# Kernel tuning notes

Hardware: AMD Instinct MI355X
Metric: run time of the kernel (lower is better)

Reference implementation:

```python
import jax, jax.numpy as jnp
import numpy as np

K_NEIGHBORS = 16  # matches init kwarg k


def _knn_idx(x, K):
    # x: (b, n, 3). Full pairwise squared distances, then top-K smallest.
    sq = jnp.sum(x * x, axis=-1)                                   # (b, n)
    d2 = sq[:, :, None] + sq[:, None, :] - 2.0 * jnp.einsum('bnc,bmc->bnm', x, x)
    _, idx = jax.lax.top_k(-d2, K)                                  # nearest first (includes self)
    return idx                                                      # (b, n, K)


def _gather(points, idx):
    # points: (b, n, C), idx: (b, n, K) -> (b, n, K, C)
    return jax.vmap(lambda p, i: p[i])(points, idx)


def _kappa_std(pc, normal, k):
    # pc, normal: (b, 3, n)
    x = pc.transpose(0, 2, 1)        # (b, n, 3)
    nrm = normal.transpose(0, 2, 1)  # (b, n, 3)
    idx = _knn_idx(x, k + 1)         # (b, n, k+1)
    nn_pts = _gather(x, idx)[:, :, 1:, :]          # drop self -> (b, n, k, 3)
    v = nn_pts - x[:, :, None, :]                   # (b, n, k, 3)
    v = v / jnp.clip(jnp.linalg.norm(v, axis=-1, keepdims=True), 1e-12)
    kappa = jnp.abs(jnp.sum(v * nrm[:, :, None, :], axis=-1)).mean(axis=-1)  # (b, n)
    nn_kappa = _gather(kappa[..., None], idx)[:, :, 1:, 0]                    # (b, n, k)
    # torch.std default: unbiased (ddof=1)
    return jnp.std(nn_kappa, axis=-1, ddof=1)                                  # (b, n)


def setup_inputs() -> dict:
    key = jax.random.key(0)
    k1, k2, k3 = jax.random.split(key, 3)
    b, n = 4, 4096
    ori_data = jax.random.normal(k1, (b, 3, n), dtype=jnp.float32)
    adv_data = ori_data + 0.05 * jax.random.normal(k2, (b, 3, n), dtype=jnp.float32)
    nrm = jax.random.normal(k3, (b, 3, n), dtype=jnp.float32)
    ori_normal = nrm / jnp.clip(jnp.linalg.norm(nrm, axis=1, keepdims=True), 1e-12)
    return {"ori_data": ori_data, "adv_data": adv_data, "ori_normal": ori_normal}


def reference(ori_data, adv_data, ori_normal):
    k = K_NEIGHBORS
    ori_std = _kappa_std(ori_data, ori_normal, k)   # (b, n)
    adv_std = _kappa_std(adv_data, ori_normal, k)   # (b, n)
    # torch PairwiseDistance(p=2, eps=1e-6): ||x1 - x2 + eps||_2 over last dim
    dist = jnp.linalg.norm(ori_std - adv_std + 1e-6, axis=-1)  # (b,)
    return dist.mean()
```

## Files before the change

kernel.cpp:

```cpp
#include <hip/hip_runtime.h>
#include <math.h>

#define NPTS 4096
#define BATCH 4
#define KNB 16
#define BIG 3.0e38f
#define CAP 1024

__device__ __forceinline__ void bsort_stage(float& d, int& s, int lane, int k, int j) {
  const float od = __shfl_xor(d, j);
  const int   os = __shfl_xor(s, j);
  const bool keepMin = ((lane & k) == 0) == ((lane & j) == 0);
  const bool takeO = keepMin ? (od < d) : (od > d);
  d = takeO ? od : d;
  s = takeO ? os : s;
}

__device__ __forceinline__ void bitonic_sort64(float& d, int& s, int lane) {
#pragma unroll
  for (int k = 2; k <= 64; k <<= 1) {
#pragma unroll
    for (int j = k >> 1; j >= 1; j >>= 1)
      bsort_stage(d, s, lane, k, j);
  }
}

__device__ __forceinline__ void bitonic_merge64(float& d, int& s, int lane) {
#pragma unroll
  for (int j = 32; j >= 1; j >>= 1)
    bsort_stage(d, s, lane, 64, j);
}

__device__ __forceinline__ void bitonic_sort64_v(float& d, int lane) {
#pragma unroll
  for (int k = 2; k <= 64; k <<= 1) {
#pragma unroll
    for (int j = k >> 1; j >= 1; j >>= 1) {
      const float od = __shfl_xor(d, j);
      const bool keepMin = ((lane & k) == 0) == ((lane & j) == 0);
      d = keepMin ? fminf(d, od) : fmaxf(d, od);
    }
  }
}

__global__ __launch_bounds__(256)
void knn_kappa_kernel(const float* __restrict__ ori,
                      const float* __restrict__ adv,
                      const float* __restrict__ nrm,
                      float* __restrict__ kappaWs,
                      int* __restrict__ idxWs) {
  const int i    = blockIdx.x;
  const int b    = blockIdx.y;
  const int ds   = blockIdx.z;
  const int t    = threadIdx.x;
  const int lane = t & 63;
  const int w    = t >> 6;

  const float* __restrict__ P  = (ds == 0 ? ori : adv) + (size_t)b * 3 * NPTS;
  const float* __restrict__ Xp = P;
  const float* __restrict__ Yp = P + NPTS;
  const float* __restrict__ Zp = P + 2 * NPTS;

  __shared__ float candD[CAP];
  __shared__ int   candI[CAP];
  __shared__ float wTau[4];
  __shared__ unsigned int cnt;

  if (t == 0) cnt = 0;

  const float xi = Xp[i], yi = Yp[i], zi = Zp[i];

  float d[16];
  float tmin = BIG;
#pragma unroll
  for (int u = 0; u < 16; ++u) {
    const int j = u * 256 + t;
    const float dx = Xp[j] - xi;
    const float dy = Yp[j] - yi;
    const float dz = Zp[j] - zi;
    float d2 = fmaf(dx, dx, fmaf(dy, dy, dz * dz));
    if (j == i) d2 = BIG;
    d[u] = d2;
    tmin = fminf(tmin, d2);
  }

  float sm = tmin;
  bitonic_sort64_v(sm, lane);
  if (lane == (KNB - 1)) wTau[w] = sm;
  __syncthreads();
  const float tau = fminf(fminf(wTau[0], wTau[1]), fminf(wTau[2], wTau[3]));

#pragma unroll
  for (int u = 0; u < 16; ++u) {
    if (d[u] <= tau) {
      const unsigned pos = atomicAdd(&cnt, 1u);
      if (pos < CAP) { candD[pos] = d[u]; candI[pos] = u * 256 + t; }
    }
  }
  __syncthreads();

  if (w == 0) {
    const int M = (int)(cnt < CAP ? cnt : CAP);
    float sd = (lane < M) ? candD[lane] : BIG;
    int   si = (lane < M) ? lane : -1;
    bitonic_sort64(sd, si, lane);
    for (int c0 = 64; c0 < M; c0 += 64) {
      const int slot = c0 + lane;
      float vd = (slot < M) ? candD[slot] : BIG;
      int   vi = (slot < M) ? slot : -1;
      bitonic_sort64(vd, vi, lane);
      const float rd = __shfl_xor(vd, 63);
      const int   ri = __shfl_xor(vi, 63);
      if (rd < sd) { sd = rd; si = ri; }
      bitonic_merge64(sd, si, lane);
    }

    if (lane < KNB) {
      const int nbj = candI[si];
      const float px = Xp[nbj], py = Yp[nbj], pz = Zp[nbj];
      const float vx = px - xi, vy = py - yi, vz = pz - zi;
      float L = sqrtf(fmaf(vx, vx, fmaf(vy, vy, vz * vz)));
      L = fmaxf(L, 1e-12f);
      const float* __restrict__ nb_ = nrm + (size_t)b * 3 * NPTS;
      const float nx = nb_[i], ny = nb_[NPTS + i], nz = nb_[2 * NPTS + i];
      float c = fabsf(fmaf(vx, nx, fmaf(vy, ny, vz * nz)) / L);
      c += __shfl_xor(c, 1);
      c += __shfl_xor(c, 2);
      c += __shfl_xor(c, 4);
      c += __shfl_xor(c, 8);
      const size_t row = (size_t)(ds * BATCH + b) * NPTS + i;
      if (lane == 0) kappaWs[row] = c * (1.0f / 16.0f);
      idxWs[row * KNB + lane] = nbj;
    }
  }
}

__global__ __launch_bounds__(256)
void std_dist_kernel(const float* __restrict__ kappaWs,
                     const int* __restrict__ idxWs,
                     float* __restrict__ partial) {
  const int i = blockIdx.x * 256 + threadIdx.x;
  const int b = blockIdx.y;

  float s[2];
#pragma unroll
  for (int ds = 0; ds < 2; ++ds) {
    const size_t kb = (size_t)(ds * BATCH + b) * NPTS;
    const int* __restrict__ ip = idxWs + (kb + i) * KNB;
    float kv[16];
    float sum = 0.f;
#pragma unroll
    for (int u = 0; u < 16; ++u) {
      kv[u] = kappaWs[kb + ip[u]];
      sum += kv[u];
    }
    const float mean = sum * (1.0f / 16.0f);
    float ss = 0.f;
#pragma unroll
    for (int u = 0; u < 16; ++u) {
      const float dv = kv[u] - mean;
      ss = fmaf(dv, dv, ss);
    }
    s[ds] = sqrtf(ss * (1.0f / 15.0f));
  }

  float dq = s[0] - s[1] + 1e-6f;
  dq = dq * dq;

  dq += __shfl_xor(dq, 32);
  dq += __shfl_xor(dq, 16);
  dq += __shfl_xor(dq, 8);
  dq += __shfl_xor(dq, 4);
  dq += __shfl_xor(dq, 2);
  dq += __shfl_xor(dq, 1);
  __shared__ float red[4];
  if ((threadIdx.x & 63) == 0) red[threadIdx.x >> 6] = dq;
  __syncthreads();
  if (threadIdx.x == 0)
    partial[b * 16 + blockIdx.x] = red[0] + red[1] + red[2] + red[3];
}

__global__ void finalize_kernel(const float* __restrict__ partial,
                                float* __restrict__ out) {
  const int l = threadIdx.x;
  float v = partial[l];
  v += __shfl_xor(v, 1);
  v += __shfl_xor(v, 2);
  v += __shfl_xor(v, 4);
  v += __shfl_xor(v, 8);
  float s = sqrtf(v);
  s += __shfl_xor(s, 16);
  s += __shfl_xor(s, 32);
  if (l == 0) out[0] = s * 0.25f;
}

extern "C" void kernel_launch(void* const* d_in, const int* in_sizes, int n_in,
                              void* d_out, int out_size, void* d_ws, size_t ws_size,
                              hipStream_t stream) {
  const float* ori = (const float*)d_in[0];
  const float* adv = (const float*)d_in[1];
  const float* nrm = (const float*)d_in[2];
  float* out = (float*)d_out;

  float* kappaWs = (float*)d_ws;
  int*   idxWs   = (int*)((char*)d_ws + (size_t)2 * BATCH * NPTS * 4);
  float* partial = (float*)((char*)d_ws + (size_t)2 * BATCH * NPTS * 4
                                        + (size_t)2 * BATCH * NPTS * KNB * 4);

  dim3 g1(NPTS, BATCH, 2);
  knn_kappa_kernel<<<g1, 256, 0, stream>>>(ori, adv, nrm, kappaWs, idxWs);

  dim3 g2(NPTS / 256, BATCH);
  std_dist_kernel<<<g2, 256, 0, stream>>>(kappaWs, idxWs, partial);

  finalize_kernel<<<dim3(1), 64, 0, stream>>>(partial, out);
}
```

Baseline: 149.6 us.

## Use radix ballot threshold, vectorized loads, and fuse finalize into std kernel

Replaces the per-wave 64-element bitonic sort that picks the candidate threshold with a 12-step bit-prefix ballot search over float bits. Point loads become float4 vectors with a contiguous per-thread index mapping. Self is no longer masked; it is instead skipped by taking sorted rank+1 after the merge. The finalize kernel is removed in favour of atomic accumulation with a last-block-done pattern, and CAP is halved to cut shared memory. This risks correctness if the coarse threshold admits more than CAP candidates or if accum is zeroed after some std block has already added to it.

```diff
diff --git a/kernel.cpp b/kernel.cpp
--- a/kernel.cpp
+++ b/kernel.cpp
@@ -5,7 +5,7 @@
 #define BATCH 4
 #define KNB 16
 #define BIG 3.0e38f
-#define CAP 1024
+#define CAP 512
 
 __device__ __forceinline__ void bsort_stage(float& d, int& s, int lane, int k, int j) {
   const float od = __shfl_xor(d, j);
@@ -31,24 +31,13 @@
     bsort_stage(d, s, lane, 64, j);
 }
 
-__device__ __forceinline__ void bitonic_sort64_v(float& d, int lane) {
-#pragma unroll
-  for (int k = 2; k <= 64; k <<= 1) {
-#pragma unroll
-    for (int j = k >> 1; j >= 1; j >>= 1) {
-      const float od = __shfl_xor(d, j);
-      const bool keepMin = ((lane & k) == 0) == ((lane & j) == 0);
-      d = keepMin ? fminf(d, od) : fmaxf(d, od);
-    }
-  }
-}
-
 __global__ __launch_bounds__(256)
 void knn_kappa_kernel(const float* __restrict__ ori,
                       const float* __restrict__ adv,
                       const float* __restrict__ nrm,
                       float* __restrict__ kappaWs,
-                      int* __restrict__ idxWs) {
+                      int* __restrict__ idxWs,
+                      float* __restrict__ accum) {
   const int i    = blockIdx.x;
   const int b    = blockIdx.y;
   const int ds   = blockIdx.z;
@@ -56,45 +45,73 @@
   const int lane = t & 63;
   const int w    = t >> 6;
 
-  const float* __restrict__ P  = (ds == 0 ? ori : adv) + (size_t)b * 3 * NPTS;
-  const float* __restrict__ Xp = P;
-  const float* __restrict__ Yp = P + NPTS;
-  const float* __restrict__ Zp = P + 2 * NPTS;
+  if (i == 0 && b == 0 && ds == 0 && t < 8) accum[t] = 0.0f;
+
+  const float* __restrict__ P = (ds == 0 ? ori : adv) + (size_t)b * 3 * NPTS;
+  const float4* __restrict__ X4 = (const float4*)(P);
+  const float4* __restrict__ Y4 = (const float4*)(P + NPTS);
+  const float4* __restrict__ Z4 = (const float4*)(P + 2 * NPTS);
 
   __shared__ float candD[CAP];
   __shared__ int   candI[CAP];
-  __shared__ float wTau[4];
+  __shared__ unsigned int wTau[4];
   __shared__ unsigned int cnt;
 
   if (t == 0) cnt = 0;
 
-  const float xi = Xp[i], yi = Yp[i], zi = Zp[i];
+  const float xi = P[i], yi = P[NPTS + i], zi = P[2 * NPTS + i];
 
   float d[16];
   float tmin = BIG;
+  const int base4 = t * 4;
+#pragma unroll
+  for (int k = 0; k < 4; ++k) {
+    const float4 xv = X4[base4 + k];
+    const float4 yv = Y4[base4 + k];
+    const float4 zv = Z4[base4 + k];
+    {
+      const float dx = xv.x - xi, dy = yv.x - yi, dz = zv.x - zi;
+      d[k * 4 + 0] = fmaf(dx, dx, fmaf(dy, dy, dz * dz));
+    }
+    {
+      const float dx = xv.y - xi, dy = yv.y - yi, dz = zv.y - zi;
+      d[k * 4 + 1] = fmaf(dx, dx, fmaf(dy, dy, dz * dz));
+    }
+    {
+      const float dx = xv.z - xi, dy = yv.z - yi, dz = zv.z - zi;
+      d[k * 4 + 2] = fmaf(dx, dx, fmaf(dy, dy, dz * dz));
+    }
+    {
+      const float dx = xv.w - xi, dy = yv.w - yi, dz = zv.w - zi;
+      d[k * 4 + 3] = fmaf(dx, dx, fmaf(dy, dy, dz * dz));
+    }
+    tmin = fminf(tmin, fminf(fminf(d[k * 4 + 0], d[k * 4 + 1]),
+                             fminf(d[k * 4 + 2], d[k * 4 + 3])));
+  }
+
+  {
+    const unsigned mb = __float_as_uint(tmin);
+    unsigned G = 0;
+#pragma unroll
+    for (int bit = 11; bit >= 0; --bit) {
+      const unsigned trial = G | (1u << bit);
+      const unsigned T = (trial << 19) | 0x7FFFFu;
+      const int c = __popcll(__ballot(mb <= T));
+      if (c < 17) G = trial;
+    }
+    unsigned T0 = (G << 19) | 0x7FFFFu;
+    const int c0 = __popcll(__ballot(mb <= T0));
+    if (c0 < 17) T0 = ((G + 1u) << 19) | 0x7FFFFu;
+    if (lane == 0) wTau[w] = T0;
+  }
+  __syncthreads();
+  const unsigned tauBits = min(min(wTau[0], wTau[1]), min(wTau[2], wTau[3]));
+
 #pragma unroll
   for (int u = 0; u < 16; ++u) {
-    const int j = u * 256 + t;
-    const float dx = Xp[j] - xi;
-    const float dy = Yp[j] - yi;
-    const float dz = Zp[j] - zi;
-    float d2 = fmaf(dx, dx, fmaf(dy, dy, dz * dz));
-    if (j == i) d2 = BIG;
-    d[u] = d2;
-    tmin = fminf(tmin, d2);
-  }
-
-  float sm = tmin;
-  bitonic_sort64_v(sm, lane);
-  if (lane == (KNB - 1)) wTau[w] = sm;
-  __syncthreads();
-  const float tau = fminf(fminf(wTau[0], wTau[1]), fminf(wTau[2], wTau[3]));
-
-#pragma unroll
-  for (int u = 0; u < 16; ++u) {
-    if (d[u] <= tau) {
+    if (__float_as_uint(d[u]) <= tauBits) {
       const unsigned pos = atomicAdd(&cnt, 1u);
-      if (pos < CAP) { candD[pos] = d[u]; candI[pos] = u * 256 + t; }
+      if (pos < CAP) { candD[pos] = d[u]; candI[pos] = t * 16 + u; }
     }
   }
   __syncthreads();
@@ -115,12 +132,13 @@
       bitonic_merge64(sd, si, lane);
     }
 
+    const int siN = __shfl(si, lane + 1);
     if (lane < KNB) {
-      const int nbj = candI[si];
-      const float px = Xp[nbj], py = Yp[nbj], pz = Zp[nbj];
-      const float vx = px - xi, vy = py - yi, vz = pz - zi;
-      float L = sqrtf(fmaf(vx, vx, fmaf(vy, vy, vz * vz)));
-      L = fmaxf(L, 1e-12f);
+      const int nbj = candI[siN];
+      const float vx = P[nbj] - xi;
+      const float vy = P[NPTS + nbj] - yi;
+      const float vz = P[2 * NPTS + nbj] - zi;
+      float L = fmaxf(sqrtf(fmaf(vx, vx, fmaf(vy, vy, vz * vz))), 1e-12f);
       const float* __restrict__ nb_ = nrm + (size_t)b * 3 * NPTS;
       const float nx = nb_[i], ny = nb_[NPTS + i], nz = nb_[2 * NPTS + i];
       float c = fabsf(fmaf(vx, nx, fmaf(vy, ny, vz * nz)) / L);
@@ -138,7 +156,8 @@
 __global__ __launch_bounds__(256)
 void std_dist_kernel(const float* __restrict__ kappaWs,
                      const int* __restrict__ idxWs,
-                     float* __restrict__ partial) {
+                     float* __restrict__ accum,
+                     float* __restrict__ out) {
   const int i = blockIdx.x * 256 + threadIdx.x;
   const int b = blockIdx.y;
 
@@ -146,14 +165,17 @@
 #pragma unroll
   for (int ds = 0; ds < 2; ++ds) {
     const size_t kb = (size_t)(ds * BATCH + b) * NPTS;
-    const int* __restrict__ ip = idxWs + (kb + i) * KNB;
+    const int4* __restrict__ ip = (const int4*)(idxWs + (kb + i) * KNB);
+    const int4 q0 = ip[0], q1 = ip[1], q2 = ip[2], q3 = ip[3];
+    const float* __restrict__ kp = kappaWs + kb;
     float kv[16];
+    kv[0] = kp[q0.x];  kv[1] = kp[q0.y];  kv[2] = kp[q0.z];  kv[3] = kp[q0.w];
+    kv[4] = kp[q1.x];  kv[5] = kp[q1.y];  kv[6] = kp[q1.z];  kv[7] = kp[q1.w];
+    kv[8] = kp[q2.x];  kv[9] = kp[q2.y];  kv[10] = kp[q2.z]; kv[11] = kp[q2.w];
+    kv[12] = kp[q3.x]; kv[13] = kp[q3.y]; kv[14] = kp[q3.z]; kv[15] = kp[q3.w];
     float sum = 0.f;
 #pragma unroll
-    for (int u = 0; u < 16; ++u) {
-      kv[u] = kappaWs[kb + ip[u]];
-      sum += kv[u];
-    }
+    for (int u = 0; u < 16; ++u) sum += kv[u];
     const float mean = sum * (1.0f / 16.0f);
     float ss = 0.f;
 #pragma unroll
@@ -176,22 +198,19 @@
   __shared__ float red[4];
   if ((threadIdx.x & 63) == 0) red[threadIdx.x >> 6] = dq;
   __syncthreads();
-  if (threadIdx.x == 0)
-    partial[b * 16 + blockIdx.x] = red[0] + red[1] + red[2] + red[3];
-}
-
-__global__ void finalize_kernel(const float* __restrict__ partial,
-                                float* __restrict__ out) {
-  const int l = threadIdx.x;
-  float v = partial[l];
-  v += __shfl_xor(v, 1);
-  v += __shfl_xor(v, 2);
-  v += __shfl_xor(v, 4);
-  v += __shfl_xor(v, 8);
-  float s = sqrtf(v);
-  s += __shfl_xor(s, 16);
-  s += __shfl_xor(s, 32);
-  if (l == 0) out[0] = s * 0.25f;
+
+  if (threadIdx.x == 0) {
+    const float blockSum = red[0] + red[1] + red[2] + red[3];
+    atomicAdd(&accum[b], blockSum);
+    __threadfence();
+    const unsigned old = atomicAdd((unsigned int*)(accum + 4), 1u);
+    if (old == 63) {
+      float ssum = 0.f;
+#pragma unroll
+      for (int bb = 0; bb < 4; ++bb) ssum += sqrtf(atomicAdd(&accum[bb], 0.0f));
+      out[0] = ssum * 0.25f;
+    }
+  }
 }
 
 extern "C" void kernel_launch(void* const* d_in, const int* in_sizes, int n_in,
@@ -204,14 +223,12 @@
 
   float* kappaWs = (float*)d_ws;
   int*   idxWs   = (int*)((char*)d_ws + (size_t)2 * BATCH * NPTS * 4);
-  float* partial = (float*)((char*)d_ws + (size_t)2 * BATCH * NPTS * 4
+  float* accum   = (float*)((char*)d_ws + (size_t)2 * BATCH * NPTS * 4
                                         + (size_t)2 * BATCH * NPTS * KNB * 4);
 
   dim3 g1(NPTS, BATCH, 2);
-  knn_kappa_kernel<<<g1, 256, 0, stream>>>(ori, adv, nrm, kappaWs, idxWs);
+  knn_kappa_kernel<<<g1, 256, 0, stream>>>(ori, adv, nrm, kappaWs, idxWs, accum);
 
   dim3 g2(NPTS / 256, BATCH);
-  std_dist_kernel<<<g2, 256, 0, stream>>>(kappaWs, idxWs, partial);
-
-  finalize_kernel<<<dim3(1), 64, 0, stream>>>(partial, out);
-}
+  std_dist_kernel<<<g2, 256, 0, stream>>>(kappaWs, idxWs, accum, out);
+}
```

Measured after the change: 157.4 us. +5.2%, slower.
